# Kernel tuning notes

Measured on AMD Instinct MI355X. Metric: run time of the kernel, lower is better.

## Reference

```python
import jax, jax.numpy as jnp
import numpy as np

N = 50000          # num vertices
K = 16             # max padded neighbors
D = 256            # feature dim
H = 256            # num_hidddens


def setup_inputs() -> dict:
    key = jax.random.key(0)
    k1, k2, k3, k4, k5 = jax.random.split(key, 5)
    vertex_feat = jax.random.normal(k1, (N, D), dtype=jnp.float32)
    neighbors_idx = jax.random.randint(k2, (N, K), 0, N, dtype=jnp.int32)
    valid_lens = jax.random.randint(k3, (N,), 0, K + 1, dtype=jnp.int32)
    W = jax.random.normal(k4, (D, H), dtype=jnp.float32) * (1.0 / np.sqrt(D))
    B = jax.random.normal(k5, (D, H), dtype=jnp.float32) * (1.0 / np.sqrt(D))
    return {"vertex_feat": vertex_feat, "neighbors_idx": neighbors_idx,
            "valid_lens": valid_lens, "W": W, "B": B}


def reference(vertex_feat, neighbors_idx, valid_lens, W, B):
    # gather neighbor features: [N, K, D]
    nb = vertex_feat[neighbors_idx]
    # sequence mask over padded neighbor slots: [N, K]
    mask = (jnp.arange(K)[None, :] < valid_lens[:, None]).astype(vertex_feat.dtype)
    # masked sum then mean (valid_lens==0 -> divide by 1, matching tf.where guard)
    agg = jnp.einsum('nkd,nk->nd', nb, mask)
    denom = jnp.maximum(valid_lens, 1).astype(vertex_feat.dtype)
    agg = agg / denom[:, None]
    # dual dense (no bias) + relu
    out = jax.nn.relu(agg @ W + vertex_feat @ B)
    return out
```

## Files before the change

kernel.cpp:

```cpp
#include <hip/hip_runtime.h>
#include <stdint.h>


#define N_V   50000
#define KNB   16
#define D_F   256
#define H_F   256
#define HK2   512
#define NPAD  50048

typedef __bf16 bf16x8 __attribute__((ext_vector_type(8)));
typedef float  f32x4  __attribute__((ext_vector_type(4)));

static __device__ __forceinline__ unsigned short f2bf(float f) {
    union { float f; unsigned u; } v; v.f = f;
    unsigned u = v.u;
    u += 0x7fffu + ((u >> 16) & 1u);
    return (unsigned short)(u >> 16);
}
static __device__ __forceinline__ float bf2f(unsigned short u) {
    union { unsigned u; float f; } v; v.u = ((unsigned)u) << 16; return v.f;
}
static __device__ __forceinline__ void load16(const void* g, void* l) {
    __builtin_amdgcn_global_load_lds(
        (__attribute__((address_space(1))) void*)g,
        (__attribute__((address_space(3))) void*)l, 16, 0, 0);
}

__global__ __launch_bounds__(256) void wbt_convert(
    const float* __restrict__ W, const float* __restrict__ Bm,
    unsigned short* __restrict__ WBt) {
    __shared__ unsigned short t[32][33];
    const int k0 = blockIdx.x * 32;
    const int h0 = blockIdx.y * 32;
    const int tid = threadIdx.x;
    {
        int r  = tid >> 3;
        int c4 = (tid & 7) * 4;
        const float* src = (h0 < 256)
            ? (W  + (size_t)(k0 + r) * H_F + h0 + c4)
            : (Bm + (size_t)(k0 + r) * H_F + (h0 - 256) + c4);
        float4 v = *(const float4*)src;
        t[r][c4 + 0] = f2bf(v.x); t[r][c4 + 1] = f2bf(v.y);
        t[r][c4 + 2] = f2bf(v.z); t[r][c4 + 3] = f2bf(v.w);
    }
    __syncthreads();
    {
        int hh  = tid >> 3;
        int kk4 = (tid & 7) * 4;
        ushort4 o;
        o.x = t[kk4 + 0][hh]; o.y = t[kk4 + 1][hh];
        o.z = t[kk4 + 2][hh]; o.w = t[kk4 + 3][hh];
        *(ushort4*)(WBt + (size_t)(h0 + hh) * D_F + k0 + kk4) = o;
    }
}

__global__ __launch_bounds__(512, 4) void gemm_y(
    const float* __restrict__ vf,
    const unsigned short* __restrict__ WBt,
    unsigned short* __restrict__ Y) {
    __shared__ char Alds[2][4096];
    __shared__ char Blds[2][32768];
    const int bm   = blockIdx.x * 64;
    const int tid  = threadIdx.x;
    const int wave = tid >> 6, lane = tid & 63;
    const int wm   = wave >> 2, wn = wave & 3;

    f32x4 acc[2][8];
    const f32x4 fzero = {0.f, 0.f, 0.f, 0.f};
#pragma unroll
    for (int i = 0; i < 2; ++i)
#pragma unroll
        for (int j = 0; j < 8; ++j) acc[i][j] = fzero;

    const int ar = tid >> 3;
    const int ak = (tid & 7) * 4;
    const int arow_g = (bm + ar < N_V) ? bm + ar : N_V - 1;
    const float* aptr = vf + (size_t)arow_g * D_F + ak;
    const unsigned aP = ar * 64u + (((unsigned)ak * 2u) ^ (((unsigned)ar & 3u) << 4));

    unsigned boff[4];
#pragma unroll
    for (int i = 0; i < 4; ++i) {
        unsigned P = i * 8192u + tid * 16u;
        unsigned L = P ^ (((P >> 6) & 3u) << 4);
        boff[i] = (L >> 6) * 512u + (L & 63u);
    }

    float4 aReg;
    auto stageA_load = [&](int t) { aReg = *(const float4*)(aptr + t * 32); };
    auto stageA_write = [&](int buf) {
        ushort4 o;
        o.x = f2bf(aReg.x); o.y = f2bf(aReg.y);
        o.z = f2bf(aReg.z); o.w = f2bf(aReg.w);
        *(ushort4*)(Alds[buf] + aP) = o;
    };
    auto stageB = [&](int buf, int t) {
#pragma unroll
        for (int i = 0; i < 4; ++i)
            load16((const char*)WBt + boff[i] + t * 64,
                   Blds[buf] + i * 8192 + wave * 1024);
    };

    stageA_load(0); stageB(0, 0); stageA_write(0);
    __syncthreads();
    int cur = 0;
    for (int t = 0; t < 8; ++t) {
        if (t < 7) { stageA_load(t + 1); stageB(cur ^ 1, t + 1); }
        bf16x8 af[2];
#pragma unroll
        for (int mf = 0; mf < 2; ++mf) {
            unsigned r = wm * 32u + mf * 16u + (lane & 15);
            unsigned c = ((unsigned)lane >> 4) << 4;
            af[mf] = *(const bf16x8*)(Alds[cur] + r * 64 + (c ^ ((r & 3u) << 4)));
        }
#pragma unroll
        for (int nf = 0; nf < 8; ++nf) {
            unsigned r = wn * 128u + nf * 16u + (lane & 15);
            unsigned c = ((unsigned)lane >> 4) << 4;
            bf16x8 bfr = *(const bf16x8*)(Blds[cur] + r * 64 + (c ^ ((r & 3u) << 4)));
            acc[0][nf] = __builtin_amdgcn_mfma_f32_16x16x32_bf16(
                af[0], bfr, acc[0][nf], 0, 0, 0);
            acc[1][nf] = __builtin_amdgcn_mfma_f32_16x16x32_bf16(
                af[1], bfr, acc[1][nf], 0, 0, 0);
        }
        if (t < 7) stageA_write(cur ^ 1);
        __syncthreads();
        cur ^= 1;
    }

#pragma unroll
    for (int mf = 0; mf < 2; ++mf) {
        int row0 = bm + wm * 32 + mf * 16 + ((lane >> 4) << 2);
#pragma unroll
        for (int nf = 0; nf < 8; ++nf) {
            int col = wn * 128 + nf * 16 + (lane & 15);
            f32x4 v = acc[mf][nf];
#pragma unroll
            for (int i = 0; i < 4; ++i)
                Y[(size_t)(row0 + i) * HK2 + col] = f2bf(v[i]);
        }
    }
}

__global__ __launch_bounds__(256) void gather_out(
    const unsigned short* __restrict__ Y, const int* __restrict__ nbr,
    const int* __restrict__ lens, float* __restrict__ out) {
    const int wave = threadIdx.x >> 6;
    const int lane = threadIdx.x & 63;
    const int n = blockIdx.x * 4 + wave;
    if (n >= N_V) return;
    const int len = lens[n];
    const int idx = nbr[(size_t)n * KNB + (lane & 15)];
    const ushort4 y2 = *(const ushort4*)(Y + (size_t)n * HK2 + 256 + lane * 4);
    f32x4 acc = {0.f, 0.f, 0.f, 0.f};
#define ROW_(j) (*(const ushort4*)(Y + (size_t)(j) * HK2 + lane * 4))
#define ACC_(v) { acc[0] += bf2f(v.x); acc[1] += bf2f(v.y); \
                  acc[2] += bf2f(v.z); acc[3] += bf2f(v.w); }
    int k = 0;
    for (; k + 4 <= len; k += 4) {
        int j0 = __shfl(idx, k),     j1 = __shfl(idx, k + 1);
        int j2 = __shfl(idx, k + 2), j3 = __shfl(idx, k + 3);
        ushort4 v0 = ROW_(j0), v1 = ROW_(j1), v2 = ROW_(j2), v3 = ROW_(j3);
        ACC_(v0); ACC_(v1); ACC_(v2); ACC_(v3);
    }
    for (; k < len; ++k) {
        int j = __shfl(idx, k);
        ushort4 v = ROW_(j);
        ACC_(v);
    }
#undef ROW_
#undef ACC_
    const float inv = 1.0f / (float)(len > 0 ? len : 1);
    float4 o;
    o.x = fmaxf(fmaf(acc[0], inv, bf2f(y2.x)), 0.f);
    o.y = fmaxf(fmaf(acc[1], inv, bf2f(y2.y)), 0.f);
    o.z = fmaxf(fmaf(acc[2], inv, bf2f(y2.z)), 0.f);
    o.w = fmaxf(fmaf(acc[3], inv, bf2f(y2.w)), 0.f);
    *(float4*)(out + (size_t)n * H_F + lane * 4) = o;
}

extern "C" void kernel_launch(void* const* d_in, const int* in_sizes, int n_in,
                              void* d_out, int out_size, void* d_ws, size_t ws_size,
                              hipStream_t stream) {
    const float* vf   = (const float*)d_in[0];
    const int*   nbr  = (const int*)d_in[1];
    const int*   lens = (const int*)d_in[2];
    const float* W    = (const float*)d_in[3];
    const float* Bm   = (const float*)d_in[4];
    float* out = (float*)d_out;

    unsigned short* Y   = (unsigned short*)d_ws;
    unsigned short* WBt = Y + (size_t)NPAD * HK2;

    hipLaunchKernelGGL(wbt_convert, dim3(8, 16), dim3(256), 0, stream, W, Bm, WBt);
    hipLaunchKernelGGL(gemm_y, dim3(NPAD / 64), dim3(512), 0, stream, vf, WBt, Y);
    hipLaunchKernelGGL(gather_out, dim3(N_V / 4), dim3(256), 0, stream,
                       Y, nbr, lens, out);
}
```

Measured before the change: 168.8 us.

## Pre-convert features to bf16, retile GEMM with resident B slab, widen gather

```diff
diff --git a/kernel.cpp b/kernel.cpp
--- a/kernel.cpp
+++ b/kernel.cpp
@@ -11,6 +11,8 @@
 
 typedef __bf16 bf16x8 __attribute__((ext_vector_type(8)));
 typedef float  f32x4  __attribute__((ext_vector_type(4)));
+typedef float  f32x8  __attribute__((ext_vector_type(8)));
+typedef unsigned short ushort8 __attribute__((ext_vector_type(8)));
 
 static __device__ __forceinline__ unsigned short f2bf(float f) {
     union { float f; unsigned u; } v; v.f = f;
@@ -25,6 +27,25 @@
     __builtin_amdgcn_global_load_lds(
         (__attribute__((address_space(1))) void*)g,
         (__attribute__((address_space(3))) void*)l, 16, 0, 0);
+}
+
+__global__ __launch_bounds__(256) void vf_convert(
+    const float* __restrict__ vf, unsigned short* __restrict__ vfb) {
+    const int total = NPAD * (D_F / 8);
+    for (int c = blockIdx.x * 256 + threadIdx.x; c < total; c += gridDim.x * 256) {
+        int n = c >> 5;
+        int off = (c & 31) * 8;
+        ushort8 o;
+        if (n < N_V) {
+            const float4 a = *(const float4*)(vf + (size_t)n * D_F + off);
+            const float4 b = *(const float4*)(vf + (size_t)n * D_F + off + 4);
+            o[0]=f2bf(a.x); o[1]=f2bf(a.y); o[2]=f2bf(a.z); o[3]=f2bf(a.w);
+            o[4]=f2bf(b.x); o[5]=f2bf(b.y); o[6]=f2bf(b.z); o[7]=f2bf(b.w);
+        } else {
+            o = (ushort8)(0);
+        }
+        *(ushort8*)(vfb + (size_t)n * D_F + off) = o;
+    }
 }
 
 __global__ __launch_bounds__(256) void wbt_convert(
@@ -56,75 +77,64 @@
 }
 
 __global__ __launch_bounds__(512, 4) void gemm_y(
-    const float* __restrict__ vf,
+    const unsigned short* __restrict__ vfb,
     const unsigned short* __restrict__ WBt,
     unsigned short* __restrict__ Y) {
-    __shared__ char Alds[2][4096];
-    __shared__ char Blds[2][32768];
-    const int bm   = blockIdx.x * 64;
-    const int tid  = threadIdx.x;
+    __shared__ char Bp[65536];
+    __shared__ char Ap[2][8192];
+    const int bn = blockIdx.x * 128;
+    const int bm = blockIdx.y * 128;
+    const int tid = threadIdx.x;
     const int wave = tid >> 6, lane = tid & 63;
-    const int wm   = wave >> 2, wn = wave & 3;
-
-    f32x4 acc[2][8];
+    const int wm = wave & 3, wn = wave >> 2;
+
+    f32x4 acc[2][4];
     const f32x4 fzero = {0.f, 0.f, 0.f, 0.f};
 #pragma unroll
     for (int i = 0; i < 2; ++i)
 #pragma unroll
-        for (int j = 0; j < 8; ++j) acc[i][j] = fzero;
-
-    const int ar = tid >> 3;
-    const int ak = (tid & 7) * 4;
-    const int arow_g = (bm + ar < N_V) ? bm + ar : N_V - 1;
-    const float* aptr = vf + (size_t)arow_g * D_F + ak;
-    const unsigned aP = ar * 64u + (((unsigned)ak * 2u) ^ (((unsigned)ar & 3u) << 4));
-
-    unsigned boff[4];
-#pragma unroll
-    for (int i = 0; i < 4; ++i) {
+        for (int j = 0; j < 4; ++j) acc[i][j] = fzero;
+
+#pragma unroll
+    for (int i = 0; i < 8; ++i) {
         unsigned P = i * 8192u + tid * 16u;
-        unsigned L = P ^ (((P >> 6) & 3u) << 4);
-        boff[i] = (L >> 6) * 512u + (L & 63u);
-    }
-
-    float4 aReg;
-    auto stageA_load = [&](int t) { aReg = *(const float4*)(aptr + t * 32); };
-    auto stageA_write = [&](int buf) {
-        ushort4 o;
-        o.x = f2bf(aReg.x); o.y = f2bf(aReg.y);
-        o.z = f2bf(aReg.z); o.w = f2bf(aReg.w);
-        *(ushort4*)(Alds[buf] + aP) = o;
+        unsigned r = P >> 9, pc = P & 511u;
+        unsigned lc = pc ^ ((r & 7u) << 4);
+        load16((const char*)WBt + (size_t)(bn + r) * 512 + lc,
+               Bp + i * 8192 + wave * 1024);
+    }
+    auto stageA = [&](int buf, int t) {
+        unsigned P = tid * 16u;
+        unsigned r = P >> 6, pc = P & 63u;
+        unsigned lc = pc ^ ((r & 3u) << 4);
+        load16((const char*)vfb + (size_t)(bm + r) * 512 + t * 64 + lc,
+               Ap[buf] + wave * 1024);
     };
-    auto stageB = [&](int buf, int t) {
-#pragma unroll
-        for (int i = 0; i < 4; ++i)
-            load16((const char*)WBt + boff[i] + t * 64,
-                   Blds[buf] + i * 8192 + wave * 1024);
-    };
-
-    stageA_load(0); stageB(0, 0); stageA_write(0);
+    stageA(0, 0);
     __syncthreads();
+
     int cur = 0;
     for (int t = 0; t < 8; ++t) {
-        if (t < 7) { stageA_load(t + 1); stageB(cur ^ 1, t + 1); }
-        bf16x8 af[2];
+        if (t < 7) stageA(cur ^ 1, t + 1);
+        bf16x8 af[2], bfr[4];
 #pragma unroll
         for (int mf = 0; mf < 2; ++mf) {
             unsigned r = wm * 32u + mf * 16u + (lane & 15);
             unsigned c = ((unsigned)lane >> 4) << 4;
-            af[mf] = *(const bf16x8*)(Alds[cur] + r * 64 + (c ^ ((r & 3u) << 4)));
-        }
-#pragma unroll
-        for (int nf = 0; nf < 8; ++nf) {
-            unsigned r = wn * 128u + nf * 16u + (lane & 15);
-            unsigned c = ((unsigned)lane >> 4) << 4;
-            bf16x8 bfr = *(const bf16x8*)(Blds[cur] + r * 64 + (c ^ ((r & 3u) << 4)));
-            acc[0][nf] = __builtin_amdgcn_mfma_f32_16x16x32_bf16(
-                af[0], bfr, acc[0][nf], 0, 0, 0);
-            acc[1][nf] = __builtin_amdgcn_mfma_f32_16x16x32_bf16(
-                af[1], bfr, acc[1][nf], 0, 0, 0);
-        }
-        if (t < 7) stageA_write(cur ^ 1);
+            af[mf] = *(const bf16x8*)(Ap[cur] + r * 64 + (c ^ ((r & 3u) << 4)));
+        }
+#pragma unroll
+        for (int nf = 0; nf < 4; ++nf) {
+            unsigned r = wn * 64u + nf * 16u + (lane & 15);
+            unsigned c = t * 64u + (((unsigned)lane >> 4) << 4);
+            bfr[nf] = *(const bf16x8*)(Bp + r * 512 + (c ^ ((r & 7u) << 4)));
+        }
+#pragma unroll
+        for (int mf = 0; mf < 2; ++mf)
+#pragma unroll
+            for (int nf = 0; nf < 4; ++nf)
+                acc[mf][nf] = __builtin_amdgcn_mfma_f32_16x16x32_bf16(
+                    af[mf], bfr[nf], acc[mf][nf], 0, 0, 0);
         __syncthreads();
         cur ^= 1;
     }
@@ -133,8 +143,8 @@
     for (int mf = 0; mf < 2; ++mf) {
         int row0 = bm + wm * 32 + mf * 16 + ((lane >> 4) << 2);
 #pragma unroll
-        for (int nf = 0; nf < 8; ++nf) {
-            int col = wn * 128 + nf * 16 + (lane & 15);
+        for (int nf = 0; nf < 4; ++nf) {
+            int col = bn + wn * 64 + nf * 16 + (lane & 15);
             f32x4 v = acc[mf][nf];
 #pragma unroll
             for (int i = 0; i < 4; ++i)
@@ -148,36 +158,47 @@
     const int* __restrict__ lens, float* __restrict__ out) {
     const int wave = threadIdx.x >> 6;
     const int lane = threadIdx.x & 63;
-    const int n = blockIdx.x * 4 + wave;
-    if (n >= N_V) return;
-    const int len = lens[n];
-    const int idx = nbr[(size_t)n * KNB + (lane & 15)];
-    const ushort4 y2 = *(const ushort4*)(Y + (size_t)n * HK2 + 256 + lane * 4);
-    f32x4 acc = {0.f, 0.f, 0.f, 0.f};
-#define ROW_(j) (*(const ushort4*)(Y + (size_t)(j) * HK2 + lane * 4))
-#define ACC_(v) { acc[0] += bf2f(v.x); acc[1] += bf2f(v.y); \
-                  acc[2] += bf2f(v.z); acc[3] += bf2f(v.w); }
+    const int half = lane >> 5, laneh = lane & 31;
+    const int v = blockIdx.x * 8 + wave * 2 + half;
+    const int base = lane & 32;
+    const int col = laneh * 8;
+
+    const int len = lens[v];
+    const int idx = nbr[(size_t)v * KNB + (laneh & 15)];
+    const ushort8 y2 = *(const ushort8*)(Y + (size_t)v * HK2 + 256 + col);
+
+    f32x8 acc = {0.f,0.f,0.f,0.f,0.f,0.f,0.f,0.f};
+#define ROW_(j) (*(const ushort8*)(Y + (size_t)(j) * HK2 + col))
+#define ACC_(r) { acc[0]+=bf2f(r[0]); acc[1]+=bf2f(r[1]); acc[2]+=bf2f(r[2]); \
+                  acc[3]+=bf2f(r[3]); acc[4]+=bf2f(r[4]); acc[5]+=bf2f(r[5]); \
+                  acc[6]+=bf2f(r[6]); acc[7]+=bf2f(r[7]); }
     int k = 0;
     for (; k + 4 <= len; k += 4) {
-        int j0 = __shfl(idx, k),     j1 = __shfl(idx, k + 1);
-        int j2 = __shfl(idx, k + 2), j3 = __shfl(idx, k + 3);
-        ushort4 v0 = ROW_(j0), v1 = ROW_(j1), v2 = ROW_(j2), v3 = ROW_(j3);
-        ACC_(v0); ACC_(v1); ACC_(v2); ACC_(v3);
+        int j0 = __shfl(idx, base + k),     j1 = __shfl(idx, base + k + 1);
+        int j2 = __shfl(idx, base + k + 2), j3 = __shfl(idx, base + k + 3);
+        ushort8 r0 = ROW_(j0), r1 = ROW_(j1), r2 = ROW_(j2), r3 = ROW_(j3);
+        ACC_(r0); ACC_(r1); ACC_(r2); ACC_(r3);
     }
     for (; k < len; ++k) {
-        int j = __shfl(idx, k);
-        ushort4 v = ROW_(j);
-        ACC_(v);
+        int j = __shfl(idx, base + k);
+        ushort8 r = ROW_(j);
+        ACC_(r);
     }
 #undef ROW_
 #undef ACC_
     const float inv = 1.0f / (float)(len > 0 ? len : 1);
-    float4 o;
-    o.x = fmaxf(fmaf(acc[0], inv, bf2f(y2.x)), 0.f);
-    o.y = fmaxf(fmaf(acc[1], inv, bf2f(y2.y)), 0.f);
-    o.z = fmaxf(fmaf(acc[2], inv, bf2f(y2.z)), 0.f);
-    o.w = fmaxf(fmaf(acc[3], inv, bf2f(y2.w)), 0.f);
-    *(float4*)(out + (size_t)n * H_F + lane * 4) = o;
+    float4 o0, o1;
+    o0.x = fmaxf(fmaf(acc[0], inv, bf2f(y2[0])), 0.f);
+    o0.y = fmaxf(fmaf(acc[1], inv, bf2f(y2[1])), 0.f);
+    o0.z = fmaxf(fmaf(acc[2], inv, bf2f(y2[2])), 0.f);
+    o0.w = fmaxf(fmaf(acc[3], inv, bf2f(y2[3])), 0.f);
+    o1.x = fmaxf(fmaf(acc[4], inv, bf2f(y2[4])), 0.f);
+    o1.y = fmaxf(fmaf(acc[5], inv, bf2f(y2[5])), 0.f);
+    o1.z = fmaxf(fmaf(acc[6], inv, bf2f(y2[6])), 0.f);
+    o1.w = fmaxf(fmaf(acc[7], inv, bf2f(y2[7])), 0.f);
+    float* op = out + (size_t)v * H_F + col;
+    *(float4*)op = o0;
+    *(float4*)(op + 4) = o1;
 }
 
 extern "C" void kernel_launch(void* const* d_in, const int* in_sizes, int n_in,
@@ -190,11 +211,14 @@
     const float* Bm   = (const float*)d_in[4];
     float* out = (float*)d_out;
 
-    unsigned short* Y   = (unsigned short*)d_ws;
-    unsigned short* WBt = Y + (size_t)NPAD * HK2;
-
+    unsigned short* Y    = (unsigned short*)d_ws;
+    unsigned short* vfb  = Y + (size_t)NPAD * HK2;
+    unsigned short* WBt  = vfb + (size_t)NPAD * D_F;
+
+    hipLaunchKernelGGL(vf_convert, dim3(2048), dim3(256), 0, stream, vf, vfb);
     hipLaunchKernelGGL(wbt_convert, dim3(8, 16), dim3(256), 0, stream, W, Bm, WBt);
-    hipLaunchKernelGGL(gemm_y, dim3(NPAD / 64), dim3(512), 0, stream, vf, WBt, Y);
-    hipLaunchKernelGGL(gather_out, dim3(N_V / 4), dim3(256), 0, stream,
+    hipLaunchKernelGGL(gemm_y, dim3(4, NPAD / 128), dim3(512), 0, stream,
+                       vfb, WBt, Y);
+    hipLaunchKernelGGL(gather_out, dim3(N_V / 8), dim3(256), 0, stream,
                        Y, nbr, lens, out);
 }
```

Measured after the change: 174.1 us. +3.1%, slower.
